# Optimization experiments

Hardware: AMD Instinct MI355X
Metric: run time of the kernel (lower is better)

The kernel has to match this reference:

```python
import jax, jax.numpy as jnp
import numpy as np

K = 8   # heads
d = 8   # per-head dim
D = K * d  # 64


def setup_inputs() -> dict:
    key = jax.random.key(0)
    ks = jax.random.split(key, 12)
    B, T, N = 8, 12, 512
    s2 = 1.0 / np.sqrt(2 * D)
    s1 = 1.0 / np.sqrt(D)
    return {
        "X": jax.random.normal(ks[0], (B, T, N, D), jnp.float32),
        "STE": jax.random.normal(ks[1], (B, T, N, D), jnp.float32),
        "W7": jax.random.uniform(ks[2], (2 * D, D), jnp.float32, -s2, s2),
        "b7": jnp.zeros((D,), jnp.float32),
        "W8": jax.random.uniform(ks[3], (2 * D, D), jnp.float32, -s2, s2),
        "b8": jnp.zeros((D,), jnp.float32),
        "W9": jax.random.uniform(ks[4], (2 * D, D), jnp.float32, -s2, s2),
        "b9": jnp.zeros((D,), jnp.float32),
        "W10": jax.random.uniform(ks[5], (D, D), jnp.float32, -s1, s1),
        "b10": jnp.zeros((D,), jnp.float32),
        "W11": jax.random.uniform(ks[6], (D, D), jnp.float32, -s1, s1),
        "b11": jnp.zeros((D,), jnp.float32),
    }


def _heads(x):
    # torch.cat(torch.split(x, d, -1), 0): [B,T,N,D] -> [K,B,T,N,d] (head-major batch)
    B, T, N, _ = x.shape
    return jnp.moveaxis(x.reshape(B, T, N, K, d), 3, 0)


def reference(X, STE, W7, b7, W8, b8, W9, b9, W10, b10, W11, b11):
    H = jnp.concatenate([X, STE], axis=-1)                 # [B,T,N,2D]
    q = _heads(jax.nn.relu(H @ W7 + b7))                   # [K,B,T,N,d]
    k = _heads(jax.nn.relu(H @ W8 + b8))
    v = _heads(jax.nn.relu(H @ W9 + b9))
    scores = jnp.einsum('kbtnd,kbtmd->kbtnm', q, k) / jnp.sqrt(jnp.float32(d))
    attn = jax.nn.softmax(scores, axis=-1)                 # [K,B,T,N,N]
    out = jnp.einsum('kbtnm,kbtmd->kbtnd', attn, v)        # [K,B,T,N,d]
    # torch.cat(torch.split(out, B, 0), -1): [K,B,T,N,d] -> [B,T,N,K*d]
    Kk, B, T, N, _ = out.shape
    out = jnp.moveaxis(out, 0, 3).reshape(B, T, N, D)
    return jax.nn.relu(out @ W10 + b10) @ W11 + b11
```

## Files before the change

### kernel.cpp

```cpp
#include <hip/hip_runtime.h>
#include <hip/hip_bf16.h>
#include <math.h>

#define BT    96
#define NSEQ  512
#define DMODEL 64
#define RTOT  (BT * NSEQ)

#define QOFF  0
#define KOFF  ((size_t)RTOT * DMODEL)
#define VOFF  ((size_t)2 * RTOT * DMODEL)
#define OOFF  ((size_t)3 * RTOT * DMODEL)
#define WOFF  ((size_t)4 * RTOT * DMODEL)

#define HPLANE ((size_t)RTOT * 8)

static __device__ inline float fast_exp2(float x) {
#if __has_builtin(__builtin_amdgcn_exp2f)
    return __builtin_amdgcn_exp2f(x);
#else
    float r; asm("v_exp_f32 %0, %1" : "=v"(r) : "v"(x)); return r;
#endif
}
static __device__ inline float fast_rcp(float x) {
#if __has_builtin(__builtin_amdgcn_rcpf)
    return __builtin_amdgcn_rcpf(x);
#else
    return 1.f / x;
#endif
}

typedef __attribute__((ext_vector_type(8)))  short short8;
typedef __attribute__((ext_vector_type(16))) float float16v;

static __device__ inline short8 as_s8(uint4 u) {
    union { uint4 u; short8 s; } x; x.u = u; return x.s;
}

static __device__ inline uint32_t bf162_bits(__hip_bfloat162 h) {
    union { __hip_bfloat162 h; uint32_t u; } x; x.h = h; return x.u;
}

static __device__ inline void split_pack8(const float* v, uint4* hi, uint4* lo) {
    uint32_t h[4], l[4];
    #pragma unroll
    for (int t = 0; t < 4; ++t) {
        float x0 = v[2 * t], x1 = v[2 * t + 1];
        uint32_t hw = bf162_bits(__float22bfloat162_rn(make_float2(x0, x1)));
        float h0 = __uint_as_float(hw << 16);
        float h1 = __uint_as_float(hw & 0xffff0000u);
        h[t] = hw;
        float l0 = x0 - h0;
        float l1 = x1 - h1;
        l[t] = bf162_bits(__float22bfloat162_rn(make_float2(l0, l1)));
    }
    *hi = make_uint4(h[0], h[1], h[2], h[3]);
    *lo = make_uint4(l[0], l[1], l[2], l[3]);
}

__global__ __launch_bounds__(256) void wprep_kernel(
    const float* __restrict__ W7, const float* __restrict__ W8,
    const float* __restrict__ W9, const float* __restrict__ W10,
    const float* __restrict__ W11,
    uint4* __restrict__ WfH, uint4* __restrict__ WfL)
{
    const int e = blockIdx.x * 256 + threadIdx.x;
    const float* W;
    int k0, col;
    if (e < 3072) {
        int n  = e & 31;
        int t  = (e >> 5) & 1;
        int hh = (e >> 6) & 1;
        int c  = (e >> 7) & 7;
        int w  = e >> 10;
        W = (w == 0) ? W7 : (w == 1) ? W8 : W9;
        k0 = c * 16 + hh * 8;
        col = t * 32 + n;
    } else {
        int pe = e - 3072;
        int n  = pe & 31;
        int t  = (pe >> 5) & 1;
        int hh = (pe >> 6) & 1;
        int c  = (pe >> 7) & 3;
        int m  = pe >> 9;
        W = (m == 0) ? W10 : W11;
        k0 = c * 16 + hh * 8;
        col = t * 32 + n;
    }
    float v[8];
    #pragma unroll
    for (int j = 0; j < 8; ++j) v[j] = W[(size_t)(k0 + j) * 64 + col];
    uint4 hi, lo;
    split_pack8(v, &hi, &lo);
    WfH[e] = hi;
    WfL[e] = lo;
}

__global__ __launch_bounds__(384) void qkv_kernel(
    const float* __restrict__ X, const float* __restrict__ STE,
    const uint4* __restrict__ WfH, const uint4* __restrict__ WfL,
    const float* __restrict__ b7, const float* __restrict__ b8,
    const float* __restrict__ b9,
    float* __restrict__ qkv)
{
    __shared__ float Xs[32][132];
    __shared__ uint4 aH[512];
    __shared__ uint4 aL[512];

    const int tid  = threadIdx.x;
    const int l31  = tid & 31;
    const int hh   = (tid >> 5) & 1;
    const int wave = tid >> 6;
    const int w    = wave >> 1;
    const int tt   = wave & 1;
    const size_t blockrow = (size_t)blockIdx.x * 32;

    for (int e = tid; e < 1024; e += 384) {
        const int row = e >> 5;
        const int seg = e & 31;
        const float* src = (seg < 16) ? X : STE;
        const float4 v = *(const float4*)(src + (blockrow + row) * 64 + (seg & 15) * 4);
        float* dst = &Xs[row][seg * 4];
        dst[0] = v.x; dst[1] = v.y; dst[2] = v.z; dst[3] = v.w;
    }
    __syncthreads();

    for (int e = tid; e < 512; e += 384) {
        const int el  = e & 31;
        const int ehh = (e >> 5) & 1;
        const int ec  = e >> 6;
        const float* hp = &Xs[el][ec * 16 + ehh * 8];
        float av[8];
        #pragma unroll
        for (int j = 0; j < 8; ++j) av[j] = hp[j];
        uint4 hi, lo;
        split_pack8(av, &hi, &lo);
        aH[e] = hi;
        aL[e] = lo;
    }
    __syncthreads();

    float16v accM, accC;
    #pragma unroll
    for (int i = 0; i < 16; ++i) { accM[i] = 0.f; accC[i] = 0.f; }

    #pragma unroll
    for (int c = 0; c < 8; ++c) {
        const uint4 ahi = aH[c * 64 + hh * 32 + l31];
        const uint4 alo = aL[c * 64 + hh * 32 + l31];
        const int ei = w * 1024 + c * 128 + hh * 64 + tt * 32 + l31;
        const uint4 bh = WfH[ei];
        const uint4 bl = WfL[ei];
        accM = __builtin_amdgcn_mfma_f32_32x32x16_bf16(
            as_s8(ahi), as_s8(bh), accM, 0, 0, 0);
        accC = __builtin_amdgcn_mfma_f32_32x32x16_bf16(
            as_s8(alo), as_s8(bh), accC, 0, 0, 0);
        accC = __builtin_amdgcn_mfma_f32_32x32x16_bf16(
            as_s8(ahi), as_s8(bl), accC, 0, 0, 0);
    }

    const float* bv = (w == 0) ? b7 : (w == 1) ? b8 : b9;
    const int head = tt * 4 + (l31 >> 3);
    const int d    = l31 & 7;
    const int col  = tt * 32 + l31;
    float* obase = qkv + (size_t)w * ((size_t)RTOT * DMODEL) + (size_t)head * HPLANE;
    const float bias = bv[col];
    #pragma unroll
    for (int r = 0; r < 16; ++r) {
        const int rowC = (r & 3) + 8 * (r >> 2) + 4 * hh;
        obase[(blockrow + rowC) * 8 + d] =
            fmaxf(accM[r] + accC[r] + bias, 0.f);
    }
}

__global__ __launch_bounds__(512, 4) void attn_kernel(
    const float* __restrict__ qkv, float* __restrict__ obuf)
{
    __shared__ uint4 ak1[16 * 32];
    __shared__ uint4 ak2p[16 * 33];
    __shared__ uint4 vfh[640];
    __shared__ uint4 vfl[640];

    const int tid  = threadIdx.x;
    const int lane = tid & 63;
    const int l31  = lane & 31;
    const int hh   = lane >> 5;
    const int wv   = tid >> 6;
    const int head = blockIdx.x & 7;
    const int bt   = blockIdx.x >> 3;

    const size_t hb = (size_t)head * HPLANE + (size_t)bt * (NSEQ * 8);
    const float* Qp = qkv + QOFF + hb;
    const float* Kp = qkv + KOFF + hb;
    const float* Vp = qkv + VOFF + hb;

    const uint4 z4 = make_uint4(0, 0, 0, 0);

    {
        const int k = tid;
        const float* kr = Kp + (size_t)k * 8;
        float kv[8];
        float4 a = *(const float4*)(kr);
        float4 b = *(const float4*)(kr + 4);
        kv[0] = a.x; kv[1] = a.y; kv[2] = a.z; kv[3] = a.w;
        kv[4] = b.x; kv[5] = b.y; kv[6] = b.z; kv[7] = b.w;
        uint4 hi, lo;
        split_pack8(kv, &hi, &lo);
        ak1[k] = hi;
        ak2p[(k >> 5) * 33 + (k & 31)] = lo;
    }
    if (tid < 16) ak2p[tid * 33 + 32] = z4;

    for (int e = tid; e < 640; e += 512) {
        if (e < 576) {
            int s  = e / 18;
            int r  = e % 18;
            int hv = r / 9;
            int n  = r % 9;
            float vv[8];
            #pragma unroll
            for (int j = 0; j < 8; ++j) {
                int key = 16 * s + ((j < 4) ? (4 * hv + j) : (8 + 4 * hv + (j - 4)));
                vv[j] = (n < 8) ? Vp[(size_t)key * 8 + n] : 1.0f;
            }
            uint4 hi, lo;
            split_pack8(vv, &hi, &lo);
            vfh[e] = hi;
            vfl[e] = lo;
        } else {
            vfh[e] = z4;
            vfl[e] = z4;
        }
    }

    __syncthreads();

    const float C = 0.51012091684045906f;
    const int idx2 = hh ? 32 : l31;

    float16v Z16;
    #pragma unroll
    for (int i = 0; i < 16; ++i) Z16[i] = 0.f;

    for (int qt = wv; qt < 16; qt += 8) {
        const float* qp = Qp + (size_t)(qt * 32 + l31) * 8;
        float qv[8];
        {
            float4 a = *(const float4*)(qp);
            float4 b = *(const float4*)(qp + 4);
            qv[0] = a.x * C; qv[1] = a.y * C; qv[2] = a.z * C; qv[3] = a.w * C;
            qv[4] = b.x * C; qv[5] = b.y * C; qv[6] = b.z * C; qv[7] = b.w * C;
        }
        uint4 qhi, qlo;
        split_pack8(qv, &qhi, &qlo);
        const uint4 bq1 = hh ? qlo : qhi;
        const uint4 bq2 = qhi;

        float16v Oa = Z16, Ob = Z16;

        for (int c = 0; c < 16; ++c) {
            const uint4 a1 = ak1[c * 32 + l31];
            const uint4 a2 = ak2p[c * 33 + idx2];

            float16v S;
            S = __builtin_amdgcn_mfma_f32_32x32x16_bf16(as_s8(a1), as_s8(bq1), Z16, 0, 0, 0);
            S = __builtin_amdgcn_mfma_f32_32x32x16_bf16(as_s8(a2), as_s8(bq2), S, 0, 0, 0);

            float pv[16];
            #pragma unroll
            for (int i = 0; i < 16; ++i) pv[i] = fast_exp2(S[i]);

            uint4 ph0, pl0, ph1, pl1;
            split_pack8(&pv[0], &ph0, &pl0);
            split_pack8(&pv[8], &ph1, &pl1);

            const int vi0 = (4 * c + hh) * 9;
            const uint4 bh0 = vfh[vi0 + l31];
            const uint4 bl0 = vfl[vi0 + l31];
            Oa = __builtin_amdgcn_mfma_f32_32x32x16_bf16(as_s8(ph0), as_s8(bh0), Oa, 0, 0, 0);
            Oa = __builtin_amdgcn_mfma_f32_32x32x16_bf16(as_s8(pl0), as_s8(bh0), Oa, 0, 0, 0);
            Oa = __builtin_amdgcn_mfma_f32_32x32x16_bf16(as_s8(ph0), as_s8(bl0), Oa, 0, 0, 0);

            const int vi1 = (4 * c + 2 + hh) * 9;
            const uint4 bh1 = vfh[vi1 + l31];
            const uint4 bl1 = vfl[vi1 + l31];
            Ob = __builtin_amdgcn_mfma_f32_32x32x16_bf16(as_s8(ph1), as_s8(bh1), Ob, 0, 0, 0);
            Ob = __builtin_amdgcn_mfma_f32_32x32x16_bf16(as_s8(pl1), as_s8(bh1), Ob, 0, 0, 0);
            Ob = __builtin_amdgcn_mfma_f32_32x32x16_bf16(as_s8(ph1), as_s8(bl1), Ob, 0, 0, 0);
        }

        #pragma unroll
        for (int r = 0; r < 16; ++r) {
            float ov = Oa[r] + Ob[r];
            float den = __uint_as_float(
                __builtin_amdgcn_ds_swizzle(__float_as_uint(ov), 0x100));
            float o = ov * fast_rcp(den);
            if (l31 < 8) {
                int row = (r & 3) + 8 * (r >> 2) + 4 * hh;
                obuf[hb + (size_t)(qt * 32 + row) * 8 + l31] = o;
            }
        }
    }
}

__global__ __launch_bounds__(128) void proj_kernel(
    const float* __restrict__ obuf,
    const uint4* __restrict__ WfH, const uint4* __restrict__ WfL,
    const float* __restrict__ b10, const float* __restrict__ b11,
    float* __restrict__ out)
{
    __shared__ float Ts[32][80];

    const int tid  = threadIdx.x;
    const int lane = tid & 63;
    const int l31  = lane & 31;
    const int hh   = lane >> 5;
    const int tw   = tid >> 6;
    const size_t row = (size_t)blockIdx.x * 32 + l31;
    const size_t blockrow = (size_t)blockIdx.x * 32;

    float16v accM, accC;
    #pragma unroll
    for (int i = 0; i < 16; ++i) { accM[i] = 0.f; accC[i] = 0.f; }

    #pragma unroll
    for (int c = 0; c < 4; ++c) {
        const float* ap = obuf + (size_t)(2 * c + hh) * HPLANE + row * 8;
        float av[8];
        {
            float4 a0 = *(const float4*)(ap);
            float4 a1 = *(const float4*)(ap + 4);
            av[0] = a0.x; av[1] = a0.y; av[2] = a0.z; av[3] = a0.w;
            av[4] = a1.x; av[5] = a1.y; av[6] = a1.z; av[7] = a1.w;
        }
        uint4 ahi, alo;
        split_pack8(av, &ahi, &alo);

        const int ei = 3072 + c * 128 + hh * 64 + tw * 32 + l31;
        const uint4 bh = WfH[ei];
        const uint4 bl = WfL[ei];
        accM = __builtin_amdgcn_mfma_f32_32x32x16_bf16(
            as_s8(ahi), as_s8(bh), accM, 0, 0, 0);
        accC = __builtin_amdgcn_mfma_f32_32x32x16_bf16(
            as_s8(alo), as_s8(bh), accC, 0, 0, 0);
        accC = __builtin_amdgcn_mfma_f32_32x32x16_bf16(
            as_s8(ahi), as_s8(bl), accC, 0, 0, 0);
    }

    {
        const int col = tw * 32 + l31;
        const float bias = b10[col];
        #pragma unroll
        for (int r = 0; r < 16; ++r) {
            const int rowC = (r & 3) + 8 * (r >> 2) + 4 * hh;
            Ts[rowC][col] = fmaxf(accM[r] + accC[r] + bias, 0.f);
        }
    }
    __syncthreads();

    #pragma unroll
    for (int i = 0; i < 16; ++i) { accM[i] = 0.f; accC[i] = 0.f; }

    #pragma unroll
    for (int c = 0; c < 4; ++c) {
        const float* ap = &Ts[l31][c * 16 + hh * 8];
        float av[8];
        {
            float4 a0 = *(const float4*)(ap);
            float4 a1 = *(const float4*)(ap + 4);
            av[0] = a0.x; av[1] = a0.y; av[2] = a0.z; av[3] = a0.w;
            av[4] = a1.x; av[5] = a1.y; av[6] = a1.z; av[7] = a1.w;
        }
        uint4 ahi, alo;
        split_pack8(av, &ahi, &alo);

        const int ei = 3584 + c * 128 + hh * 64 + tw * 32 + l31;
        const uint4 bh = WfH[ei];
        const uint4 bl = WfL[ei];
        accM = __builtin_amdgcn_mfma_f32_32x32x16_bf16(
            as_s8(ahi), as_s8(bh), accM, 0, 0, 0);
        accC = __builtin_amdgcn_mfma_f32_32x32x16_bf16(
            as_s8(alo), as_s8(bh), accC, 0, 0, 0);
        accC = __builtin_amdgcn_mfma_f32_32x32x16_bf16(
            as_s8(ahi), as_s8(bl), accC, 0, 0, 0);
    }

    {
        const int col = tw * 32 + l31;
        const float bias = b11[col];
        #pragma unroll
        for (int r = 0; r < 16; ++r) {
            const int rowC = (r & 3) + 8 * (r >> 2) + 4 * hh;
            out[(blockrow + rowC) * 64 + col] = accM[r] + accC[r] + bias;
        }
    }
}

extern "C" void kernel_launch(void* const* d_in, const int* in_sizes, int n_in,
                              void* d_out, int out_size, void* d_ws, size_t ws_size,
                              hipStream_t stream)
{
    const float* X   = (const float*)d_in[0];
    const float* STE = (const float*)d_in[1];
    const float* W7  = (const float*)d_in[2];
    const float* b7  = (const float*)d_in[3];
    const float* W8  = (const float*)d_in[4];
    const float* b8  = (const float*)d_in[5];
    const float* W9  = (const float*)d_in[6];
    const float* b9  = (const float*)d_in[7];
    const float* W10 = (const float*)d_in[8];
    const float* b10 = (const float*)d_in[9];
    const float* W11 = (const float*)d_in[10];
    const float* b11 = (const float*)d_in[11];

    float* ws  = (float*)d_ws;
    float* out = (float*)d_out;

    uint4* WfH = (uint4*)(ws + WOFF);
    uint4* WfL = WfH + 4096;

    wprep_kernel<<<dim3(16), 256, 0, stream>>>(W7, W8, W9, W10, W11, WfH, WfL);
    qkv_kernel<<<dim3(RTOT / 32), 384, 0, stream>>>(X, STE, WfH, WfL, b7, b8, b9, ws);
    attn_kernel<<<dim3(BT * 8), 512, 0, stream>>>(ws, ws + OOFF);
    proj_kernel<<<dim3(RTOT / 32), 128, 0, stream>>>(ws + OOFF, WfH, WfL, b10, b11, out);
}
```

Measured before the change: 173.8 us.

## Split attention query tiles across two blocks and stage QKV stores through LDS

The attention kernel now launches twice as many blocks, with each block handling half of the 16 query tiles, so each wave processes one tile instead of looping over two. This spreads work across more CUs, but each block repeats the K/V load and bf16 split into shared memory. The QKV kernel now writes its MFMA outputs to shared memory reused from the input buffers, then stores them to the head-major layout as coalesced float4 writes instead of scattered scalar stores. The proj kernel's LDS row padding also changes from 80 to 84.

```diff
diff --git a/kernel.cpp b/kernel.cpp
--- a/kernel.cpp
+++ b/kernel.cpp
@@ -103,9 +103,11 @@
     const float* __restrict__ b9,
     float* __restrict__ qkv)
 {
-    __shared__ float Xs[32][132];
-    __shared__ uint4 aH[512];
-    __shared__ uint4 aL[512];
+    __shared__ __align__(16) char smem[33280];
+    float (*Xs)[132] = (float(*)[132])smem;
+    uint4* aH = (uint4*)(smem + 16896);
+    uint4* aL = (uint4*)(smem + 25088);
+    float* Tst = (float*)smem;
 
     const int tid  = threadIdx.x;
     const int l31  = tid & 31;
@@ -160,16 +162,34 @@
     }
 
     const float* bv = (w == 0) ? b7 : (w == 1) ? b8 : b9;
-    const int head = tt * 4 + (l31 >> 3);
-    const int d    = l31 & 7;
     const int col  = tt * 32 + l31;
-    float* obase = qkv + (size_t)w * ((size_t)RTOT * DMODEL) + (size_t)head * HPLANE;
     const float bias = bv[col];
+
+    __syncthreads();
     #pragma unroll
     for (int r = 0; r < 16; ++r) {
         const int rowC = (r & 3) + 8 * (r >> 2) + 4 * hh;
-        obase[(blockrow + rowC) * 8 + d] =
+        Tst[wave * 1152 + rowC * 36 + l31] =
             fmaxf(accM[r] + accC[r] + bias, 0.f);
+    }
+    __syncthreads();
+
+    #pragma unroll
+    for (int k = 0; k < 4; ++k) {
+        const int fid  = tid + k * 384;
+        const int w2   = fid >> 9;
+        const int rem  = fid & 511;
+        const int hd   = rem >> 6;
+        const int rem2 = rem & 63;
+        const int row  = rem2 >> 1;
+        const int d    = (rem2 & 1) * 4;
+        const int cc   = hd * 8 + d;
+        const int wv2  = w2 * 2 + (cc >> 5);
+        const int ct   = cc & 31;
+        const float4 v = *(const float4*)&Tst[wv2 * 1152 + row * 36 + ct];
+        float* gp = qkv + (size_t)w2 * ((size_t)RTOT * DMODEL)
+                    + (size_t)hd * HPLANE + (blockrow + row) * 8 + d;
+        *(float4*)gp = v;
     }
 }
 
@@ -186,8 +206,12 @@
     const int l31  = lane & 31;
     const int hh   = lane >> 5;
     const int wv   = tid >> 6;
-    const int head = blockIdx.x & 7;
-    const int bt   = blockIdx.x >> 3;
+    const int bx   = blockIdx.x;
+    const int qhalf = (bx >= 768) ? 1 : 0;
+    const int pid  = bx - qhalf * 768;
+    const int head = pid & 7;
+    const int bt   = pid >> 3;
+    const int qt   = qhalf * 8 + wv;
 
     const size_t hb = (size_t)head * HPLANE + (size_t)bt * (NSEQ * 8);
     const float* Qp = qkv + QOFF + hb;
@@ -242,7 +266,7 @@
     #pragma unroll
     for (int i = 0; i < 16; ++i) Z16[i] = 0.f;
 
-    for (int qt = wv; qt < 16; qt += 8) {
+    {
         const float* qp = Qp + (size_t)(qt * 32 + l31) * 8;
         float qv[8];
         {
@@ -266,13 +290,12 @@
             S = __builtin_amdgcn_mfma_f32_32x32x16_bf16(as_s8(a1), as_s8(bq1), Z16, 0, 0, 0);
             S = __builtin_amdgcn_mfma_f32_32x32x16_bf16(as_s8(a2), as_s8(bq2), S, 0, 0, 0);
 
-            float pv[16];
             #pragma unroll
-            for (int i = 0; i < 16; ++i) pv[i] = fast_exp2(S[i]);
+            for (int i = 0; i < 16; ++i) S[i] = fast_exp2(S[i]);
 
             uint4 ph0, pl0, ph1, pl1;
-            split_pack8(&pv[0], &ph0, &pl0);
-            split_pack8(&pv[8], &ph1, &pl1);
+            split_pack8((const float*)&S, &ph0, &pl0);
+            split_pack8(((const float*)&S) + 8, &ph1, &pl1);
 
             const int vi0 = (4 * c + hh) * 9;
             const uint4 bh0 = vfh[vi0 + l31];
@@ -309,7 +332,7 @@
     const float* __restrict__ b10, const float* __restrict__ b11,
     float* __restrict__ out)
 {
-    __shared__ float Ts[32][80];
+    __shared__ float Ts[32][84];
 
     const int tid  = threadIdx.x;
     const int lane = tid & 63;
@@ -421,6 +444,6 @@
 
     wprep_kernel<<<dim3(16), 256, 0, stream>>>(W7, W8, W9, W10, W11, WfH, WfL);
     qkv_kernel<<<dim3(RTOT / 32), 384, 0, stream>>>(X, STE, WfH, WfL, b7, b8, b9, ws);
-    attn_kernel<<<dim3(BT * 8), 512, 0, stream>>>(ws, ws + OOFF);
+    attn_kernel<<<dim3(BT * 8 * 2), 512, 0, stream>>>(ws, ws + OOFF);
     proj_kernel<<<dim3(RTOT / 32), 128, 0, stream>>>(ws + OOFF, WfH, WfL, b10, b11, out);
 }
```

Result: no change. 174.2 us (+0.2%).

## Split attention query tiles across two blocks and stage V through shared memory

Applied to the files above, without the earlier changes.

The attention grid is doubled so each (batch-time, head) pair is handled by two blocks, with each wave processing one query tile instead of looping over two. V is first loaded coalesced into a raw shared-memory buffer, and the strided split-pack reads now come from there instead of scattered global loads. Other changes are small: exp results are written back into the MFMA accumulator to save registers, and the proj kernel's shared tile row is padded to 84 floats. The trade-off is that K/V staging and bf16 splitting are duplicated across the two blocks, and the extra 16KB of shared memory may lower occupancy.

```diff
diff --git a/kernel.cpp b/kernel.cpp
--- a/kernel.cpp
+++ b/kernel.cpp
@@ -180,14 +180,19 @@
     __shared__ uint4 ak2p[16 * 33];
     __shared__ uint4 vfh[640];
     __shared__ uint4 vfl[640];
+    __shared__ float vraw[4096];
 
     const int tid  = threadIdx.x;
     const int lane = tid & 63;
     const int l31  = lane & 31;
     const int hh   = lane >> 5;
     const int wv   = tid >> 6;
-    const int head = blockIdx.x & 7;
-    const int bt   = blockIdx.x >> 3;
+    const int bx   = blockIdx.x;
+    const int qhalf = (bx >= 768) ? 1 : 0;
+    const int pid  = bx - qhalf * 768;
+    const int head = pid & 7;
+    const int bt   = pid >> 3;
+    const int qt   = qhalf * 8 + wv;
 
     const size_t hb = (size_t)head * HPLANE + (size_t)bt * (NSEQ * 8);
     const float* Qp = qkv + QOFF + hb;
@@ -211,6 +216,16 @@
     }
     if (tid < 16) ak2p[tid * 33 + 32] = z4;
 
+    {
+        const float* vr = Vp + (size_t)tid * 8;
+        const float4 a = *(const float4*)(vr);
+        const float4 b = *(const float4*)(vr + 4);
+        float* dst = &vraw[tid * 8];
+        dst[0] = a.x; dst[1] = a.y; dst[2] = a.z; dst[3] = a.w;
+        dst[4] = b.x; dst[5] = b.y; dst[6] = b.z; dst[7] = b.w;
+    }
+    __syncthreads();
+
     for (int e = tid; e < 640; e += 512) {
         if (e < 576) {
             int s  = e / 18;
@@ -221,7 +236,7 @@
             #pragma unroll
             for (int j = 0; j < 8; ++j) {
                 int key = 16 * s + ((j < 4) ? (4 * hv + j) : (8 + 4 * hv + (j - 4)));
-                vv[j] = (n < 8) ? Vp[(size_t)key * 8 + n] : 1.0f;
+                vv[j] = (n < 8) ? vraw[key * 8 + n] : 1.0f;
             }
             uint4 hi, lo;
             split_pack8(vv, &hi, &lo);
@@ -242,7 +257,7 @@
     #pragma unroll
     for (int i = 0; i < 16; ++i) Z16[i] = 0.f;
 
-    for (int qt = wv; qt < 16; qt += 8) {
+    {
         const float* qp = Qp + (size_t)(qt * 32 + l31) * 8;
         float qv[8];
         {
@@ -266,13 +281,12 @@
             S = __builtin_amdgcn_mfma_f32_32x32x16_bf16(as_s8(a1), as_s8(bq1), Z16, 0, 0, 0);
             S = __builtin_amdgcn_mfma_f32_32x32x16_bf16(as_s8(a2), as_s8(bq2), S, 0, 0, 0);
 
-            float pv[16];
             #pragma unroll
-            for (int i = 0; i < 16; ++i) pv[i] = fast_exp2(S[i]);
+            for (int i = 0; i < 16; ++i) S[i] = fast_exp2(S[i]);
 
             uint4 ph0, pl0, ph1, pl1;
-            split_pack8(&pv[0], &ph0, &pl0);
-            split_pack8(&pv[8], &ph1, &pl1);
+            split_pack8((const float*)&S, &ph0, &pl0);
+            split_pack8(((const float*)&S) + 8, &ph1, &pl1);
 
             const int vi0 = (4 * c + hh) * 9;
             const uint4 bh0 = vfh[vi0 + l31];
@@ -309,7 +323,7 @@
     const float* __restrict__ b10, const float* __restrict__ b11,
     float* __restrict__ out)
 {
-    __shared__ float Ts[32][80];
+    __shared__ float Ts[32][84];
 
     const int tid  = threadIdx.x;
     const int lane = tid & 63;
@@ -421,6 +435,6 @@
 
     wprep_kernel<<<dim3(16), 256, 0, stream>>>(W7, W8, W9, W10, W11, WfH, WfL);
     qkv_kernel<<<dim3(RTOT / 32), 384, 0, stream>>>(X, STE, WfH, WfL, b7, b8, b9, ws);
-    attn_kernel<<<dim3(BT * 8), 512, 0, stream>>>(ws, ws + OOFF);
+    attn_kernel<<<dim3(BT * 8 * 2), 512, 0, stream>>>(ws, ws + OOFF);
     proj_kernel<<<dim3(RTOT / 32), 128, 0, stream>>>(ws + OOFF, WfH, WfL, b10, b11, out);
 }
```

Measured after the change: 174.9 us. Within noise of the previous version (+0.6%).

## Process two query tiles per wave, drop P low-part MFMA, single accumulator chain

Applied to the files above, without the earlier changes.

The attention loop now handles both query tiles of each wave at once, so each K/V shared-memory load feeds twice the MFMA work and the two independent chains give more instruction-level parallelism. The low bf16 part of the exp probabilities is dropped, cutting PV MFMAs from 6 to 4 per tile-chunk per query tile. The Oa/Ob split becomes a single four-MFMA chain per query tile. Occupancy hint in launch_bounds is removed and proj_kernel shared-memory padding changes from 80 to 84; the dropped P low part lowers precision and the extra accumulators raise register pressure.

```diff
diff --git a/kernel.cpp b/kernel.cpp
--- a/kernel.cpp
+++ b/kernel.cpp
@@ -56,6 +56,14 @@
     }
     *hi = make_uint4(h[0], h[1], h[2], h[3]);
     *lo = make_uint4(l[0], l[1], l[2], l[3]);
+}
+
+static __device__ inline uint4 pack_hi8(const float* v) {
+    uint32_t h[4];
+    #pragma unroll
+    for (int t = 0; t < 4; ++t)
+        h[t] = bf162_bits(__float22bfloat162_rn(make_float2(v[2 * t], v[2 * t + 1])));
+    return make_uint4(h[0], h[1], h[2], h[3]);
 }
 
 __global__ __launch_bounds__(256) void wprep_kernel(
@@ -173,7 +181,7 @@
     }
 }
 
-__global__ __launch_bounds__(512, 4) void attn_kernel(
+__global__ __launch_bounds__(512) void attn_kernel(
     const float* __restrict__ qkv, float* __restrict__ obuf)
 {
     __shared__ uint4 ak1[16 * 32];
@@ -242,62 +250,92 @@
     #pragma unroll
     for (int i = 0; i < 16; ++i) Z16[i] = 0.f;
 
-    for (int qt = wv; qt < 16; qt += 8) {
-        const float* qp = Qp + (size_t)(qt * 32 + l31) * 8;
-        float qv[8];
+    {
+        const int qtA = wv;
+        const int qtB = wv + 8;
+
+        uint4 qAhi, qAlo, qBhi, qBlo;
         {
+            const float* qp = Qp + (size_t)(qtA * 32 + l31) * 8;
             float4 a = *(const float4*)(qp);
             float4 b = *(const float4*)(qp + 4);
-            qv[0] = a.x * C; qv[1] = a.y * C; qv[2] = a.z * C; qv[3] = a.w * C;
-            qv[4] = b.x * C; qv[5] = b.y * C; qv[6] = b.z * C; qv[7] = b.w * C;
-        }
-        uint4 qhi, qlo;
-        split_pack8(qv, &qhi, &qlo);
-        const uint4 bq1 = hh ? qlo : qhi;
-        const uint4 bq2 = qhi;
-
-        float16v Oa = Z16, Ob = Z16;
+            float qv[8] = { a.x * C, a.y * C, a.z * C, a.w * C,
+                            b.x * C, b.y * C, b.z * C, b.w * C };
+            split_pack8(qv, &qAhi, &qAlo);
+        }
+        {
+            const float* qp = Qp + (size_t)(qtB * 32 + l31) * 8;
+            float4 a = *(const float4*)(qp);
+            float4 b = *(const float4*)(qp + 4);
+            float qv[8] = { a.x * C, a.y * C, a.z * C, a.w * C,
+                            b.x * C, b.y * C, b.z * C, b.w * C };
+            split_pack8(qv, &qBhi, &qBlo);
+        }
+        const uint4 bqA1 = hh ? qAlo : qAhi;
+        const uint4 bqA2 = qAhi;
+        const uint4 bqB1 = hh ? qBlo : qBhi;
+        const uint4 bqB2 = qBhi;
+
+        float16v OA = Z16, OB = Z16;
 
         for (int c = 0; c < 16; ++c) {
             const uint4 a1 = ak1[c * 32 + l31];
             const uint4 a2 = ak2p[c * 33 + idx2];
 
-            float16v S;
-            S = __builtin_amdgcn_mfma_f32_32x32x16_bf16(as_s8(a1), as_s8(bq1), Z16, 0, 0, 0);
-            S = __builtin_amdgcn_mfma_f32_32x32x16_bf16(as_s8(a2), as_s8(bq2), S, 0, 0, 0);
-
-            float pv[16];
+            float16v SA, SB;
+            SA = __builtin_amdgcn_mfma_f32_32x32x16_bf16(as_s8(a1), as_s8(bqA1), Z16, 0, 0, 0);
+            SA = __builtin_amdgcn_mfma_f32_32x32x16_bf16(as_s8(a2), as_s8(bqA2), SA, 0, 0, 0);
+            SB = __builtin_amdgcn_mfma_f32_32x32x16_bf16(as_s8(a1), as_s8(bqB1), Z16, 0, 0, 0);
+            SB = __builtin_amdgcn_mfma_f32_32x32x16_bf16(as_s8(a2), as_s8(bqB2), SB, 0, 0, 0);
+
             #pragma unroll
-            for (int i = 0; i < 16; ++i) pv[i] = fast_exp2(S[i]);
-
-            uint4 ph0, pl0, ph1, pl1;
-            split_pack8(&pv[0], &ph0, &pl0);
-            split_pack8(&pv[8], &ph1, &pl1);
+            for (int i = 0; i < 16; ++i) SA[i] = fast_exp2(SA[i]);
+            #pragma unroll
+            for (int i = 0; i < 16; ++i) SB[i] = fast_exp2(SB[i]);
+
+            const uint4 phA0 = pack_hi8((const float*)&SA);
+            const uint4 phA1 = pack_hi8(((const float*)&SA) + 8);
+            const uint4 phB0 = pack_hi8((const float*)&SB);
+            const uint4 phB1 = pack_hi8(((const float*)&SB) + 8);
 
             const int vi0 = (4 * c + hh) * 9;
+            const int vi1 = (4 * c + 2 + hh) * 9;
             const uint4 bh0 = vfh[vi0 + l31];
             const uint4 bl0 = vfl[vi0 + l31];
-            Oa = __builtin_amdgcn_mfma_f32_32x32x16_bf16(as_s8(ph0), as_s8(bh0), Oa, 0, 0, 0);
-            Oa = __builtin_amdgcn_mfma_f32_32x32x16_bf16(as_s8(pl0), as_s8(bh0), Oa, 0, 0, 0);
-            Oa = __builtin_amdgcn_mfma_f32_32x32x16_bf16(as_s8(ph0), as_s8(bl0), Oa, 0, 0, 0);
-
-            const int vi1 = (4 * c + 2 + hh) * 9;
             const uint4 bh1 = vfh[vi1 + l31];
             const uint4 bl1 = vfl[vi1 + l31];
-            Ob = __builtin_amdgcn_mfma_f32_32x32x16_bf16(as_s8(ph1), as_s8(bh1), Ob, 0, 0, 0);
-            Ob = __builtin_amdgcn_mfma_f32_32x32x16_bf16(as_s8(pl1), as_s8(bh1), Ob, 0, 0, 0);
-            Ob = __builtin_amdgcn_mfma_f32_32x32x16_bf16(as_s8(ph1), as_s8(bl1), Ob, 0, 0, 0);
+
+            OA = __builtin_amdgcn_mfma_f32_32x32x16_bf16(as_s8(phA0), as_s8(bh0), OA, 0, 0, 0);
+            OA = __builtin_amdgcn_mfma_f32_32x32x16_bf16(as_s8(phA0), as_s8(bl0), OA, 0, 0, 0);
+            OA = __builtin_amdgcn_mfma_f32_32x32x16_bf16(as_s8(phA1), as_s8(bh1), OA, 0, 0, 0);
+            OA = __builtin_amdgcn_mfma_f32_32x32x16_bf16(as_s8(phA1), as_s8(bl1), OA, 0, 0, 0);
+
+            OB = __builtin_amdgcn_mfma_f32_32x32x16_bf16(as_s8(phB0), as_s8(bh0), OB, 0, 0, 0);
+            OB = __builtin_amdgcn_mfma_f32_32x32x16_bf16(as_s8(phB0), as_s8(bl0), OB, 0, 0, 0);
+            OB = __builtin_amdgcn_mfma_f32_32x32x16_bf16(as_s8(phB1), as_s8(bh1), OB, 0, 0, 0);
+            OB = __builtin_amdgcn_mfma_f32_32x32x16_bf16(as_s8(phB1), as_s8(bl1), OB, 0, 0, 0);
         }
 
         #pragma unroll
         for (int r = 0; r < 16; ++r) {
-            float ov = Oa[r] + Ob[r];
+            float ov = OA[r];
             float den = __uint_as_float(
                 __builtin_amdgcn_ds_swizzle(__float_as_uint(ov), 0x100));
             float o = ov * fast_rcp(den);
             if (l31 < 8) {
                 int row = (r & 3) + 8 * (r >> 2) + 4 * hh;
-                obuf[hb + (size_t)(qt * 32 + row) * 8 + l31] = o;
+                obuf[hb + (size_t)(qtA * 32 + row) * 8 + l31] = o;
+            }
+        }
+        #pragma unroll
+        for (int r = 0; r < 16; ++r) {
+            float ov = OB[r];
+            float den = __uint_as_float(
+                __builtin_amdgcn_ds_swizzle(__float_as_uint(ov), 0x100));
+            float o = ov * fast_rcp(den);
+            if (l31 < 8) {
+                int row = (r & 3) + 8 * (r >> 2) + 4 * hh;
+                obuf[hb + (size_t)(qtB * 32 + row) * 8 + l31] = o;
             }
         }
     }
@@ -309,7 +347,7 @@
     const float* __restrict__ b10, const float* __restrict__ b11,
     float* __restrict__ out)
 {
-    __shared__ float Ts[32][80];
+    __shared__ float Ts[32][84];
 
     const int tid  = threadIdx.x;
     const int lane = tid & 63;
```

After: 158.3 us. 1.1x faster.
